# Performance work log

Measured on AMD Instinct MI355X. Metric: run time of the kernel, lower is better.

## Reference

```python
import jax, jax.numpy as jnp
import numpy as np

# Inner-product factors for Cl(1,3) (Minkowski metric diag(+,-,-,-)).
# For blade e_b, <~e_b e_b>_0 = product of the metric signs of its constituent vectors.
# Blade order: [1, e0,e1,e2,e3, e01,e02,e03,e12,e13,e23, e012,e013,e023,e123, e0123]
_IPF = jnp.array([1, 1, -1, -1, -1, -1, -1, -1, 1, 1, 1, 1, 1, 1, -1, -1], dtype=jnp.float32)

B, H, N, CMV, CS = 4, 8, 2048, 8, 16


def setup_inputs() -> dict:
    key = jax.random.key(0)
    ks = jax.random.split(key, 6)
    f = lambda k, s: jax.random.normal(k, s, dtype=jnp.float32)
    return {
        "q_mv": f(ks[0], (B, H, N, CMV, 16)),
        "k_mv": f(ks[1], (B, H, N, CMV, 16)),
        "v_mv": f(ks[2], (B, H, N, CMV, 16)),
        "q_s": f(ks[3], (B, H, N, CS)),
        "k_s": f(ks[4], (B, H, N, CS)),
        "v_s": f(ks[5], (B, H, N, CS)),
    }


def reference(q_mv, k_mv, v_mv, q_s, k_s, v_s):
    b, h, n, cmv, _ = q_mv.shape
    cs = q_s.shape[-1]
    cmv_out = v_mv.shape[-2]
    cs_out = v_s.shape[-1]
    # GA inner product on mv part = euclidean dot after applying metric factors to queries
    q = jnp.concatenate([(q_mv * _IPF).reshape(b, h, n, cmv * 16), q_s], axis=-1)
    k = jnp.concatenate([k_mv.reshape(b, h, n, cmv * 16), k_s], axis=-1)
    v = jnp.concatenate([v_mv.reshape(b, h, n, cmv_out * 16), v_s], axis=-1)
    scale = 1.0 / np.sqrt(q.shape[-1]).astype(np.float32)  # torch SDPA default scale
    scores = jnp.einsum("bhid,bhjd->bhij", q, k) * scale  # [B,H,N,N]
    attn = jax.nn.softmax(scores, axis=-1)
    out = jnp.einsum("bhij,bhjd->bhid", attn, v)
    out_mv = out[..., : cmv_out * 16].reshape(b, h, n, cmv_out, 16)
    out_s = out[..., cmv_out * 16 : cmv_out * 16 + cs_out]
    return out_mv, out_s
```

## Files before the change

kernel.cpp:

```cpp
#include <hip/hip_runtime.h>
#include <cstdint>
#include <math.h>


#define BH    32
#define N_    2048
#define DMV   128
#define DS    16
#define D_    144
#define BM    128
#define BN    64
#define NKIT  (N_ / BN)
#define PSTR  72
#define KTILE_E  10240
#define VTILE_E  9216
#define KP_BYTES ((size_t)BH * NKIT * KTILE_E * 2)
#define QSCALE 0.12022458674074693f

typedef __bf16 bf16_8 __attribute__((ext_vector_type(8)));
typedef float  f32x4  __attribute__((ext_vector_type(4)));

#define GLOAD_LDS16(g, l)                                                     \
  __builtin_amdgcn_global_load_lds(                                           \
      (const __attribute__((address_space(1))) void*)(g),                     \
      (__attribute__((address_space(3))) void*)(l), 16, 0, 0)

__device__ __forceinline__ f32x4 mfma16(bf16_8 a, bf16_8 b, f32x4 c) {
  return __builtin_amdgcn_mfma_f32_16x16x32_bf16(a, b, c, 0, 0, 0);
}

__global__ __launch_bounds__(256)
void pack_k(const float* __restrict__ kmv, const float* __restrict__ ks_,
            __bf16* __restrict__ kp) {
  const int tile = blockIdx.x;
  const int t = threadIdx.x;
  __bf16* dst = kp + (size_t)tile * KTILE_E;
#pragma unroll
  for (int u = 0; u < 5; ++u) {
    int c = t + 256 * u;
    int f = c >> 6, r = c & 63;
    int nt = f / 5, ks = f - nt * 5;
    int quad = r >> 4, l15 = r & 15;
    int n = tile * 64 + nt * 16 + l15;
    int k = ks * 32 + quad * 8;
    bf16_8 o;
    if (k < DMV) {
      const f32x4* p = (const f32x4*)(kmv + (size_t)n * DMV + k);
      f32x4 a = p[0], b = p[1];
#pragma unroll
      for (int j = 0; j < 8; ++j) o[j] = (__bf16)((j < 4) ? a[j] : b[j - 4]);
    } else if (k < D_) {
      const f32x4* p = (const f32x4*)(ks_ + (size_t)n * DS + (k - DMV));
      f32x4 a = p[0], b = p[1];
#pragma unroll
      for (int j = 0; j < 8; ++j) o[j] = (__bf16)((j < 4) ? a[j] : b[j - 4]);
    } else {
#pragma unroll
      for (int j = 0; j < 8; ++j) o[j] = (__bf16)0.0f;
    }
    *(bf16_8*)(dst + (size_t)c * 8) = o;
  }
}

#define TSTR 156
__global__ __launch_bounds__(256)
void pack_vt(const float* __restrict__ vmv, const float* __restrict__ vs,
             __bf16* __restrict__ vt) {
  __shared__ __bf16 sT[64 * TSTR];
  const int tile = blockIdx.x;
  const int t = threadIdx.x;
  {
    const int n = t >> 2, c4 = t & 3;
    const float* mv = vmv + (size_t)(tile * 64 + n) * DMV;
    const float* s  = vs  + (size_t)(tile * 64 + n) * DS;
    __bf16* row = &sT[n * TSTR];
    if (c4 < 3) {
#pragma unroll
      for (int i = 0; i < 9; ++i) {
        f32x4 x = *(const f32x4*)(mv + c4 * 36 + 4 * i);
#pragma unroll
        for (int j = 0; j < 4; ++j) row[c4 * 36 + 4 * i + j] = (__bf16)x[j];
      }
    } else {
#pragma unroll
      for (int i = 0; i < 5; ++i) {
        f32x4 x = *(const f32x4*)(mv + 108 + 4 * i);
#pragma unroll
        for (int j = 0; j < 4; ++j) row[108 + 4 * i + j] = (__bf16)x[j];
      }
#pragma unroll
      for (int i = 0; i < 4; ++i) {
        f32x4 x = *(const f32x4*)(s + 4 * i);
#pragma unroll
        for (int j = 0; j < 4; ++j) row[128 + 4 * i + j] = (__bf16)x[j];
      }
    }
  }
  __syncthreads();
  __bf16* dst = vt + (size_t)tile * VTILE_E;
  for (int c = t; c < 1152; c += 256) {
    int f = c >> 6, r = c & 63;
    int n9 = f >> 1, ks = f & 1;
    int quad = r >> 4, l15 = r & 15;
    int d = n9 * 16 + l15;
    int n0 = ks * 32 + quad * 8;
    bf16_8 o;
#pragma unroll
    for (int j = 0; j < 8; ++j) o[j] = sT[(n0 + j) * TSTR + d];
    *(bf16_8*)(dst + (size_t)c * 8) = o;
  }
}

__device__ __forceinline__ bf16_8 load_q_frag(const float* qmv_row, const float* qs_row, int k0) {
  bf16_8 f;
  if (k0 < DMV) {
    const f32x4* p = (const f32x4*)(qmv_row + k0);
    f32x4 a = p[0], b = p[1];
    int hi = k0 & 8;
#pragma unroll
    for (int j = 0; j < 8; ++j) {
      float v = (j < 4) ? a[j] : b[j - 4];
      bool pos = hi ? (j < 6) : (j < 2);
      f[j] = (__bf16)(v * (pos ? QSCALE : -QSCALE));
    }
  } else if (k0 < D_) {
    const f32x4* p = (const f32x4*)(qs_row + (k0 - DMV));
    f32x4 a = p[0], b = p[1];
#pragma unroll
    for (int j = 0; j < 8; ++j) {
      float v = (j < 4) ? a[j] : b[j - 4];
      f[j] = (__bf16)(v * QSCALE);
    }
  } else {
#pragma unroll
    for (int j = 0; j < 8; ++j) f[j] = (__bf16)0.0f;
  }
  return f;
}

__global__ __launch_bounds__(256, 3)
void geo_attn_kernel(const float* __restrict__ q_mv, const float* __restrict__ q_s,
                     const __bf16* __restrict__ kp, const __bf16* __restrict__ vt,
                     float* __restrict__ out)
{
  __shared__ __bf16 sK[KTILE_E];
  __shared__ __bf16 sVT[VTILE_E];

  const int tid  = threadIdx.x;
  const int w    = tid >> 6;
  const int lane = tid & 63;
  const int l15  = lane & 15;
  const int quad = lane >> 4;
  const int bh    = blockIdx.y;
  const int qbase = blockIdx.x * BM;
  const size_t bh_n = (size_t)bh * N_;

  __bf16* sPw = sK + w * (32 * PSTR);

  bf16_8 qf[2][5];
#pragma unroll
  for (int rg = 0; rg < 2; ++rg) {
    int mrow = qbase + 32 * w + 16 * rg + l15;
    const float* qmv_row = q_mv + (bh_n + mrow) * DMV;
    const float* qs_row  = q_s  + (bh_n + mrow) * DS;
#pragma unroll
    for (int ks = 0; ks < 5; ++ks)
      qf[rg][ks] = load_q_frag(qmv_row, qs_row, ks * 32 + quad * 8);
  }

  f32x4 of[2][9];
#pragma unroll
  for (int rg = 0; rg < 2; ++rg)
#pragma unroll
    for (int n9 = 0; n9 < 9; ++n9)
#pragma unroll
      for (int r = 0; r < 4; ++r) of[rg][n9][r] = 0.0f;
  float m_i[2] = {-INFINITY, -INFINITY}, l_i[2] = {0.0f, 0.0f};

  const __bf16* kbase = kp + (size_t)bh * NKIT * KTILE_E;
  const __bf16* vbase = vt + (size_t)bh * NKIT * VTILE_E;

  for (int it = 0; it < NKIT; ++it) {
    {
      const __bf16* kt = kbase + (size_t)it * KTILE_E;
      const __bf16* vp = vbase + (size_t)it * VTILE_E;
      for (int i = w; i < 20; i += 4)
        GLOAD_LDS16(kt + i * 512 + lane * 8, &sK[i * 512 + lane * 8]);
      for (int i = w; i < 18; i += 4)
        GLOAD_LDS16(vp + i * 512 + lane * 8, &sVT[i * 512 + lane * 8]);
    }
    __syncthreads();

    f32x4 sf[2][4];
#pragma unroll
    for (int rg = 0; rg < 2; ++rg)
#pragma unroll
      for (int nt = 0; nt < 4; ++nt)
#pragma unroll
        for (int r = 0; r < 4; ++r) sf[rg][nt][r] = 0.0f;
#pragma unroll
    for (int ks = 0; ks < 5; ++ks) {
#pragma unroll
      for (int nt = 0; nt < 4; ++nt) {
        bf16_8 kb = *(const bf16_8*)&sK[(nt * 5 + ks) * 512 + lane * 8];
        sf[0][nt] = mfma16(kb, qf[0][ks], sf[0][nt]);
        sf[1][nt] = mfma16(kb, qf[1][ks], sf[1][nt]);
      }
    }
    __syncthreads();

#pragma unroll
    for (int rg = 0; rg < 2; ++rg) {
      float mx = sf[rg][0][0];
#pragma unroll
      for (int nt = 0; nt < 4; ++nt)
#pragma unroll
        for (int r = 0; r < 4; ++r) mx = fmaxf(mx, sf[rg][nt][r]);
      mx = fmaxf(mx, __shfl_xor(mx, 16));
      mx = fmaxf(mx, __shfl_xor(mx, 32));
      float mnew = fmaxf(m_i[rg], mx);
      float al = __builtin_amdgcn_exp2f(m_i[rg] - mnew);
      m_i[rg] = mnew;
      float rs = 0.0f;
#pragma unroll
      for (int nt = 0; nt < 4; ++nt)
#pragma unroll
        for (int r = 0; r < 4; ++r) {
          float p = __builtin_amdgcn_exp2f(sf[rg][nt][r] - mnew);
          sf[rg][nt][r] = p;
          rs += p;
        }
      rs += __shfl_xor(rs, 16);
      rs += __shfl_xor(rs, 32);
      l_i[rg] = l_i[rg] * al + rs;

#pragma unroll
      for (int nt = 0; nt < 4; ++nt) {
        __bf16 pw[4];
#pragma unroll
        for (int r = 0; r < 4; ++r) pw[r] = (__bf16)sf[rg][nt][r];
        *(uint64_t*)&sPw[(rg * 16 + l15) * PSTR + nt * 16 + quad * 4] = *(uint64_t*)pw;
      }

      float alr[4];
#pragma unroll
      for (int r = 0; r < 4; ++r) alr[r] = __shfl(al, 20 * quad + r);
#pragma unroll
      for (int n9 = 0; n9 < 9; ++n9)
#pragma unroll
        for (int r = 0; r < 4; ++r) of[rg][n9][r] *= alr[r];
    }
    asm volatile("s_waitcnt lgkmcnt(0)" ::: "memory");

#pragma unroll
    for (int ks = 0; ks < 2; ++ks) {
      bf16_8 pa[2];
#pragma unroll
      for (int rg = 0; rg < 2; ++rg)
        pa[rg] = *(const bf16_8*)&sPw[(rg * 16 + l15) * PSTR + ks * 32 + quad * 8];
#pragma unroll
      for (int n9 = 0; n9 < 9; ++n9) {
        bf16_8 vb = *(const bf16_8*)&sVT[(n9 * 2 + ks) * 512 + lane * 8];
        of[0][n9] = mfma16(pa[0], vb, of[0][n9]);
        of[1][n9] = mfma16(pa[1], vb, of[1][n9]);
      }
    }
    __syncthreads();
  }

  float* out_mv = out;
  float* out_s  = out + (size_t)BH * N_ * DMV;
#pragma unroll
  for (int rg = 0; rg < 2; ++rg) {
    float linv[4];
#pragma unroll
    for (int r = 0; r < 4; ++r)
      linv[r] = __builtin_amdgcn_rcpf(__shfl(l_i[rg], 20 * quad + r));
#pragma unroll
    for (int n9 = 0; n9 < 9; ++n9) {
#pragma unroll
      for (int r = 0; r < 4; ++r) {
        int row = qbase + 32 * w + 16 * rg + quad * 4 + r;
        float val = of[rg][n9][r] * linv[r];
        if (n9 < 8) out_mv[(bh_n + row) * DMV + n9 * 16 + l15] = val;
        else        out_s [(bh_n + row) * DS + l15] = val;
      }
    }
  }
}

extern "C" void kernel_launch(void* const* d_in, const int* in_sizes, int n_in,
                              void* d_out, int out_size, void* d_ws, size_t ws_size,
                              hipStream_t stream) {
  (void)in_sizes; (void)n_in; (void)out_size; (void)ws_size;
  const float* q_mv = (const float*)d_in[0];
  const float* k_mv = (const float*)d_in[1];
  const float* v_mv = (const float*)d_in[2];
  const float* q_s  = (const float*)d_in[3];
  const float* k_s  = (const float*)d_in[4];
  const float* v_s  = (const float*)d_in[5];
  float* out = (float*)d_out;

  __bf16* kp = (__bf16*)d_ws;
  __bf16* vt = (__bf16*)((char*)d_ws + KP_BYTES);

  pack_k<<<BH * NKIT, 256, 0, stream>>>(k_mv, k_s, kp);
  pack_vt<<<BH * NKIT, 256, 0, stream>>>(v_mv, v_s, vt);

  dim3 grid(N_ / BM, BH);
  geo_attn_kernel<<<grid, 256, 0, stream>>>(q_mv, q_s, kp, vt, out);
}
```

Measured before the change: 296.5 us.

## Split each KV tile across wave pairs with cross-wave softmax merge

```diff
diff --git a/kernel.cpp b/kernel.cpp
--- a/kernel.cpp
+++ b/kernel.cpp
@@ -8,10 +8,10 @@
 #define DMV   128
 #define DS    16
 #define D_    144
-#define BM    128
+#define BM    64
 #define BN    64
 #define NKIT  (N_ / BN)
-#define PSTR  72
+#define PSTR2 40
 #define KTILE_E  10240
 #define VTILE_E  9216
 #define KP_BYTES ((size_t)BH * NKIT * KTILE_E * 2)
@@ -143,24 +143,29 @@
                      const __bf16* __restrict__ kp, const __bf16* __restrict__ vt,
                      float* __restrict__ out)
 {
-  __shared__ __bf16 sK[KTILE_E];
-  __shared__ __bf16 sVT[VTILE_E];
+  __shared__ __align__(16) unsigned char smem[20480 + 18432 + 1024];
+  __bf16* sK  = (__bf16*)smem;
+  __bf16* sVT = (__bf16*)(smem + 20480);
+  float2* sX  = (float2*)(smem + 38912);
+  float*  sM  = (float*)smem;
 
   const int tid  = threadIdx.x;
   const int w    = tid >> 6;
   const int lane = tid & 63;
   const int l15  = lane & 15;
   const int quad = lane >> 4;
+  const int g    = w >> 1;
+  const int c    = w & 1;
   const int bh    = blockIdx.y;
   const int qbase = blockIdx.x * BM;
   const size_t bh_n = (size_t)bh * N_;
 
-  __bf16* sPw = sK + w * (32 * PSTR);
+  __bf16* sPw = sK + w * (32 * PSTR2);
 
   bf16_8 qf[2][5];
 #pragma unroll
   for (int rg = 0; rg < 2; ++rg) {
-    int mrow = qbase + 32 * w + 16 * rg + l15;
+    int mrow = qbase + 32 * g + 16 * rg + l15;
     const float* qmv_row = q_mv + (bh_n + mrow) * DMV;
     const float* qs_row  = q_s  + (bh_n + mrow) * DS;
 #pragma unroll
@@ -191,57 +196,65 @@
     }
     __syncthreads();
 
-    f32x4 sf[2][4];
+    f32x4 sf[2][2];
 #pragma unroll
     for (int rg = 0; rg < 2; ++rg)
 #pragma unroll
-      for (int nt = 0; nt < 4; ++nt)
-#pragma unroll
-        for (int r = 0; r < 4; ++r) sf[rg][nt][r] = 0.0f;
+      for (int nt2 = 0; nt2 < 2; ++nt2)
+#pragma unroll
+        for (int r = 0; r < 4; ++r) sf[rg][nt2][r] = 0.0f;
 #pragma unroll
     for (int ks = 0; ks < 5; ++ks) {
 #pragma unroll
-      for (int nt = 0; nt < 4; ++nt) {
-        bf16_8 kb = *(const bf16_8*)&sK[(nt * 5 + ks) * 512 + lane * 8];
-        sf[0][nt] = mfma16(kb, qf[0][ks], sf[0][nt]);
-        sf[1][nt] = mfma16(kb, qf[1][ks], sf[1][nt]);
-      }
-    }
-    __syncthreads();
-
+      for (int nt2 = 0; nt2 < 2; ++nt2) {
+        bf16_8 kb = *(const bf16_8*)&sK[((2 * c + nt2) * 5 + ks) * 512 + lane * 8];
+        sf[0][nt2] = mfma16(kb, qf[0][ks], sf[0][nt2]);
+        sf[1][nt2] = mfma16(kb, qf[1][ks], sf[1][nt2]);
+      }
+    }
+
+    float pmx[2], ps[2];
 #pragma unroll
     for (int rg = 0; rg < 2; ++rg) {
       float mx = sf[rg][0][0];
 #pragma unroll
-      for (int nt = 0; nt < 4; ++nt)
-#pragma unroll
-        for (int r = 0; r < 4; ++r) mx = fmaxf(mx, sf[rg][nt][r]);
+      for (int nt2 = 0; nt2 < 2; ++nt2)
+#pragma unroll
+        for (int r = 0; r < 4; ++r) mx = fmaxf(mx, sf[rg][nt2][r]);
       mx = fmaxf(mx, __shfl_xor(mx, 16));
       mx = fmaxf(mx, __shfl_xor(mx, 32));
-      float mnew = fmaxf(m_i[rg], mx);
-      float al = __builtin_amdgcn_exp2f(m_i[rg] - mnew);
-      m_i[rg] = mnew;
       float rs = 0.0f;
 #pragma unroll
-      for (int nt = 0; nt < 4; ++nt)
+      for (int nt2 = 0; nt2 < 2; ++nt2)
 #pragma unroll
         for (int r = 0; r < 4; ++r) {
-          float p = __builtin_amdgcn_exp2f(sf[rg][nt][r] - mnew);
-          sf[rg][nt][r] = p;
-          rs += p;
+          float e = __builtin_amdgcn_exp2f(sf[rg][nt2][r] - mx);
+          sf[rg][nt2][r] = e;
+          rs += e;
         }
       rs += __shfl_xor(rs, 16);
       rs += __shfl_xor(rs, 32);
-      l_i[rg] = l_i[rg] * al + rs;
-
-#pragma unroll
-      for (int nt = 0; nt < 4; ++nt) {
+      pmx[rg] = mx; ps[rg] = rs;
+      if (quad == 0) sX[((g * 2 + rg) * 2 + c) * 16 + l15] = make_float2(mx, rs);
+    }
+    __syncthreads();
+
+#pragma unroll
+    for (int rg = 0; rg < 2; ++rg) {
+      float2 ot = sX[((g * 2 + rg) * 2 + (1 - c)) * 16 + l15];
+      float mnew = fmaxf(m_i[rg], fmaxf(pmx[rg], ot.x));
+      float al  = __builtin_amdgcn_exp2f(m_i[rg] - mnew);
+      float scm = __builtin_amdgcn_exp2f(pmx[rg] - mnew);
+      float sco = __builtin_amdgcn_exp2f(ot.x - mnew);
+      l_i[rg] = l_i[rg] * al + ps[rg] * scm + ot.y * sco;
+      m_i[rg] = mnew;
+#pragma unroll
+      for (int nt2 = 0; nt2 < 2; ++nt2) {
         __bf16 pw[4];
 #pragma unroll
-        for (int r = 0; r < 4; ++r) pw[r] = (__bf16)sf[rg][nt][r];
-        *(uint64_t*)&sPw[(rg * 16 + l15) * PSTR + nt * 16 + quad * 4] = *(uint64_t*)pw;
-      }
-
+        for (int r = 0; r < 4; ++r) pw[r] = (__bf16)(sf[rg][nt2][r] * scm);
+        *(uint64_t*)&sPw[(rg * 16 + l15) * PSTR2 + nt2 * 16 + quad * 4] = *(uint64_t*)pw;
+      }
       float alr[4];
 #pragma unroll
       for (int r = 0; r < 4; ++r) alr[r] = __shfl(al, 20 * quad + r);
@@ -252,17 +265,14 @@
     }
     asm volatile("s_waitcnt lgkmcnt(0)" ::: "memory");
 
-#pragma unroll
-    for (int ks = 0; ks < 2; ++ks) {
-      bf16_8 pa[2];
-#pragma unroll
-      for (int rg = 0; rg < 2; ++rg)
-        pa[rg] = *(const bf16_8*)&sPw[(rg * 16 + l15) * PSTR + ks * 32 + quad * 8];
+    {
+      bf16_8 pa0 = *(const bf16_8*)&sPw[l15 * PSTR2 + quad * 8];
+      bf16_8 pa1 = *(const bf16_8*)&sPw[(16 + l15) * PSTR2 + quad * 8];
 #pragma unroll
       for (int n9 = 0; n9 < 9; ++n9) {
-        bf16_8 vb = *(const bf16_8*)&sVT[(n9 * 2 + ks) * 512 + lane * 8];
-        of[0][n9] = mfma16(pa[0], vb, of[0][n9]);
-        of[1][n9] = mfma16(pa[1], vb, of[1][n9]);
+        bf16_8 vb = *(const bf16_8*)&sVT[(n9 * 2 + c) * 512 + lane * 8];
+        of[0][n9] = mfma16(pa0, vb, of[0][n9]);
+        of[1][n9] = mfma16(pa1, vb, of[1][n9]);
       }
     }
     __syncthreads();
@@ -272,18 +282,30 @@
   float* out_s  = out + (size_t)BH * N_ * DMV;
 #pragma unroll
   for (int rg = 0; rg < 2; ++rg) {
-    float linv[4];
-#pragma unroll
-    for (int r = 0; r < 4; ++r)
-      linv[r] = __builtin_amdgcn_rcpf(__shfl(l_i[rg], 20 * quad + r));
-#pragma unroll
-    for (int n9 = 0; n9 < 9; ++n9) {
-#pragma unroll
-      for (int r = 0; r < 4; ++r) {
-        int row = qbase + 32 * w + 16 * rg + quad * 4 + r;
-        float val = of[rg][n9][r] * linv[r];
-        if (n9 < 8) out_mv[(bh_n + row) * DMV + n9 * 16 + l15] = val;
-        else        out_s [(bh_n + row) * DS + l15] = val;
+    __syncthreads();
+    if (c == 1) {
+#pragma unroll
+      for (int n9 = 0; n9 < 9; ++n9)
+#pragma unroll
+        for (int r = 0; r < 4; ++r)
+          sM[(g * 16 + quad * 4 + r) * 148 + n9 * 16 + l15] = of[rg][n9][r];
+    }
+    __syncthreads();
+    if (c == 0) {
+      float linv[4];
+#pragma unroll
+      for (int r = 0; r < 4; ++r)
+        linv[r] = __builtin_amdgcn_rcpf(__shfl(l_i[rg], 20 * quad + r));
+#pragma unroll
+      for (int n9 = 0; n9 < 9; ++n9) {
+#pragma unroll
+        for (int r = 0; r < 4; ++r) {
+          int row = qbase + 32 * g + 16 * rg + quad * 4 + r;
+          float val = (of[rg][n9][r] +
+                       sM[(g * 16 + quad * 4 + r) * 148 + n9 * 16 + l15]) * linv[r];
+          if (n9 < 8) out_mv[(bh_n + row) * DMV + n9 * 16 + l15] = val;
+          else        out_s [(bh_n + row) * DS + l15] = val;
+        }
       }
     }
   }
```

Result: slower. 312.3 us (+5.3%).
